# Kernel optimization log

Hardware: AMD Instinct MI355X
Metric: run time of the kernel (lower is better)

The kernel has to match this reference:

```python
import jax, jax.numpy as jnp
import numpy as np

TEMPERATURE = 0.07
EPS = 1e-12  # F.normalize clamp


def _project(x, We, be, W1, b1, W2, b2):
    # encoder Linear then projection head Linear->ReLU->Linear
    h = x @ We + be                      # [B, 512]
    h = jax.nn.relu(h @ W1 + b1)         # [B, 256]
    return h @ W2 + b2                   # [B, 128]


def _ntxent(z1, z2, t):
    B = z1.shape[0]
    z1 = z1 / jnp.maximum(jnp.linalg.norm(z1, axis=1, keepdims=True), EPS)
    z2 = z2 / jnp.maximum(jnp.linalg.norm(z2, axis=1, keepdims=True), EPS)
    reps = jnp.concatenate([z1, z2], axis=0)          # [2B, 128]
    sim = reps @ reps.T                               # [2B, 2B]
    N = 2 * B
    idx = jnp.arange(N)
    # positives: eye rolled by B along columns -> column (i+B) mod N
    pos = sim[idx, (idx + B) % N][:, None]            # [N, 1]
    # negatives: all off-diagonal entries per row, in column order
    cols = jnp.arange(N - 1)[None, :]                 # [1, N-1]
    neg_idx = cols + (cols >= idx[:, None])           # skip the diagonal
    neg = jnp.take_along_axis(sim, neg_idx, axis=1)   # [N, N-1]
    logits = jnp.concatenate([pos, neg], axis=1) / t  # [N, N]
    # cross-entropy with label 0
    return jnp.mean(jax.nn.logsumexp(logits, axis=1) - logits[:, 0])


def setup_inputs() -> dict:
    key = jax.random.key(0)
    ks = jax.random.split(key, 10)
    B, Din, Denc, Dh, Dp = 4096, 1024, 512, 256, 128
    s = lambda fan_in: 1.0 / np.sqrt(fan_in)
    return {
        "x_image": jax.random.normal(ks[0], (B, Din), jnp.float32),
        "x_text": jax.random.normal(ks[1], (B, Din), jnp.float32),
        "We_img": jax.random.normal(ks[2], (Din, Denc), jnp.float32) * s(Din),
        "be_img": jnp.zeros((Denc,), jnp.float32),
        "We_txt": jax.random.normal(ks[3], (Din, Denc), jnp.float32) * s(Din),
        "be_txt": jnp.zeros((Denc,), jnp.float32),
        "Wp1_img": jax.random.normal(ks[4], (Denc, Dh), jnp.float32) * s(Denc),
        "bp1_img": jnp.zeros((Dh,), jnp.float32),
        "Wp2_img": jax.random.normal(ks[5], (Dh, Dp), jnp.float32) * s(Dh),
        "bp2_img": jnp.zeros((Dp,), jnp.float32),
        "Wp1_txt": jax.random.normal(ks[6], (Denc, Dh), jnp.float32) * s(Denc),
        "bp1_txt": jnp.zeros((Dh,), jnp.float32),
        "Wp2_txt": jax.random.normal(ks[7], (Dh, Dp), jnp.float32) * s(Dh),
        "bp2_txt": jnp.zeros((Dp,), jnp.float32),
    }


def reference(x_image, x_text, We_img, be_img, We_txt, be_txt,
              Wp1_img, bp1_img, Wp2_img, bp2_img,
              Wp1_txt, bp1_txt, Wp2_txt, bp2_txt):
    z1 = _project(x_image, We_img, be_img, Wp1_img, bp1_img, Wp2_img, bp2_img)
    z2 = _project(x_text, We_txt, be_txt, Wp1_txt, bp1_txt, Wp2_txt, bp2_txt)
    # single modality pair ('image','text') -> one NT-Xent loss
    return _ntxent(z1, z2, TEMPERATURE)
```

## Files before the change

kernel.cpp:

```cpp
#include <hip/hip_runtime.h>
#include <hip/hip_bf16.h>
#include <math.h>

typedef __bf16 bf16_t;
typedef __bf16 bf8 __attribute__((ext_vector_type(8)));
typedef __bf16 bf4 __attribute__((ext_vector_type(4)));
typedef __bf16 bf16x2 __attribute__((ext_vector_type(2)));
typedef float f32x4 __attribute__((ext_vector_type(4)));

#define AS1 __attribute__((address_space(1)))
#define AS3 __attribute__((address_space(3)))

#define B_ROWS 4096
#define NTOT   8192
#define DIN    1024
#define DENC   512
#define DH     256
#define DP     128
#define NSLICE 16
#define INV_T        14.285714285714286f
#define SCALE_LOG2   20.609929155556620f

__device__ __forceinline__ f32x4 mfma_16x16x32(bf8 a, bf8 b, f32x4 c) {
  return __builtin_amdgcn_mfma_f32_16x16x32_bf16(a, b, c, 0, 0, 0);
}

__global__ __launch_bounds__(256) void prep_kernel(
    const float* __restrict__ x_i, const float* __restrict__ x_t,
    const float* __restrict__ We_i, const float* __restrict__ We_t,
    const float* __restrict__ W1_i, const float* __restrict__ W1_t,
    const float* __restrict__ W2_i, const float* __restrict__ W2_t,
    bf16_t* __restrict__ xb_i, bf16_t* __restrict__ xb_t,
    bf16_t* __restrict__ Wet_i, bf16_t* __restrict__ Wet_t,
    bf16_t* __restrict__ W1t_i, bf16_t* __restrict__ W1t_t,
    bf16_t* __restrict__ W2t_i, bf16_t* __restrict__ W2t_t,
    int* __restrict__ Ctr) {
  const int b = blockIdx.x;
  const int tid = threadIdx.x;
  if (b >= 336) {
    int idx = (b - 336) * 256 + tid;
    const int HALF = (B_ROWS * DIN) / 4;
    const float* s; bf16_t* d; int off;
    if (idx < HALF) { s = x_i; d = xb_i; off = idx; }
    else            { s = x_t; d = xb_t; off = idx - HALF; }
    float4 v = ((const float4*)s)[off];
    bf4 w = { (bf16_t)v.x, (bf16_t)v.y, (bf16_t)v.z, (bf16_t)v.w };
    ((bf4*)d)[off] = w;
    return;
  }
  if (b == 0 && tid < 2) Ctr[tid] = 0;
  const float* src; bf16_t* dst; int K, N, tile;
  if (b < 128)      { src = We_i; dst = Wet_i; K = 1024; N = 512; tile = b; }
  else if (b < 256) { src = We_t; dst = Wet_t; K = 1024; N = 512; tile = b - 128; }
  else if (b < 288) { src = W1_i; dst = W1t_i; K = 512;  N = 256; tile = b - 256; }
  else if (b < 320) { src = W1_t; dst = W1t_t; K = 512;  N = 256; tile = b - 288; }
  else if (b < 328) { src = W2_i; dst = W2t_i; K = 256;  N = 128; tile = b - 320; }
  else              { src = W2_t; dst = W2t_t; K = 256;  N = 128; tile = b - 328; }
  const int tilesN = N >> 6;
  const int k0 = (tile / tilesN) * 64;
  const int n0 = (tile % tilesN) * 64;

  __shared__ float ld[64][65];
  #pragma unroll
  for (int i = 0; i < 4; ++i) {
    int cid = tid + i * 256;
    int r = cid >> 4;
    int c = (cid & 15) * 4;
    float4 v = *(const float4*)(src + (size_t)(k0 + r) * N + n0 + c);
    ld[r][c + 0] = v.x; ld[r][c + 1] = v.y; ld[r][c + 2] = v.z; ld[r][c + 3] = v.w;
  }
  __syncthreads();
  #pragma unroll
  for (int i = 0; i < 2; ++i) {
    int cid = tid + i * 256;
    int rn = cid >> 3;
    int c8 = (cid & 7) * 8;
    bf8 w;
    #pragma unroll
    for (int j = 0; j < 8; ++j) w[j] = (bf16_t)ld[c8 + j][rn];
    *(bf8*)(dst + (size_t)(n0 + rn) * K + k0 + c8) = w;
  }
}

template<int MT, bool RELU>
__global__ __launch_bounds__(256) void gemm_glds(
    const bf16_t* __restrict__ A0, const bf16_t* __restrict__ A1,
    const bf16_t* __restrict__ B0, const bf16_t* __restrict__ B1,
    const float* __restrict__ bias0, const float* __restrict__ bias1,
    bf16_t* __restrict__ out0, bf16_t* __restrict__ out1,
    int N, int K) {
  const bf16_t* A   = blockIdx.z ? A1 : A0;
  const bf16_t* Bt  = blockIdx.z ? B1 : B0;
  const float* bias = blockIdx.z ? bias1 : bias0;
  bf16_t* outp      = blockIdx.z ? out1 : out0;

  const int nb   = blockIdx.x * 64;
  const int mb   = blockIdx.y * MT;
  const int tid  = threadIdx.x;
  const int wave = tid >> 6;
  const int lane = tid & 63;
  const int l15  = lane & 15;
  const int quad = lane >> 4;
  constexpr int CH = MT / 64;

  __shared__ __align__(16) bf16_t As[2][MT * 32];
  __shared__ __align__(16) bf16_t Bs[2][64 * 32];

  f32x4 acc[CH][4];
  #pragma unroll
  for (int i = 0; i < CH; ++i)
    #pragma unroll
    for (int j = 0; j < 4; ++j) acc[i][j] = (f32x4){0.f, 0.f, 0.f, 0.f};

  auto stage = [&](int k0, int pb) {
    #pragma unroll
    for (int i = 0; i < CH; ++i) {
      const int s = tid + i * 256;
      const bf16_t* ga = A + (size_t)(mb + (s >> 2)) * K + k0 + (s & 3) * 8;
      __builtin_amdgcn_global_load_lds(
          (const AS1 void*)ga,
          (AS3 void*)(As[pb] + (size_t)(wave * 64 + i * 256) * 8), 16, 0, 0);
    }
    const bf16_t* gb = Bt + (size_t)(nb + (tid >> 2)) * K + k0 + (tid & 3) * 8;
    __builtin_amdgcn_global_load_lds(
        (const AS1 void*)gb,
        (AS3 void*)(Bs[pb] + (size_t)(wave * 64) * 8), 16, 0, 0);
  };

  stage(0, 0);
  const int T = K >> 5;
  for (int t = 0; t < T; ++t) {
    __syncthreads();
    if (t + 1 < T) stage((t + 1) << 5, (t + 1) & 1);
    const bf16_t* as = As[t & 1];
    const bf16_t* bs = Bs[t & 1];
    bf8 a[CH];
    #pragma unroll
    for (int i = 0; i < CH; ++i)
      a[i] = *(const bf8*)(as + (size_t)(wave * (16 * CH) + i * 16 + l15) * 32 + quad * 8);
    #pragma unroll
    for (int nt = 0; nt < 4; ++nt) {
      bf8 bb = *(const bf8*)(bs + (size_t)(nt * 16 + l15) * 32 + quad * 8);
      #pragma unroll
      for (int i = 0; i < CH; ++i)
        acc[i][nt] = mfma_16x16x32(a[i], bb, acc[i][nt]);
    }
  }

  #pragma unroll
  for (int i = 0; i < CH; ++i) {
    const int orow = mb + wave * (16 * CH) + i * 16 + quad * 4;
    #pragma unroll
    for (int nt = 0; nt < 4; ++nt) {
      const int ocol = nb + nt * 16 + l15;
      const float bval = bias[ocol];
      #pragma unroll
      for (int r = 0; r < 4; ++r) {
        float v = acc[i][nt][r] + bval;
        if (RELU) v = fmaxf(v, 0.f);
        outp[(size_t)(orow + r) * N + ocol] = (bf16_t)v;
      }
    }
  }
}

__global__ __launch_bounds__(256) void head2_norm(
    const bf16_t* __restrict__ A0, const bf16_t* __restrict__ A1,
    const bf16_t* __restrict__ B0, const bf16_t* __restrict__ B1,
    const float* __restrict__ bias0, const float* __restrict__ bias1,
    bf16_t* __restrict__ reps) {
  const bf16_t* A   = blockIdx.z ? A1 : A0;
  const bf16_t* Bt  = blockIdx.z ? B1 : B0;
  const float* bias = blockIdx.z ? bias1 : bias0;

  const int mb   = blockIdx.x * 16;
  const int tid  = threadIdx.x;
  const int wave = tid >> 6;
  const int lane = tid & 63;
  const int l15  = lane & 15;
  const int quad = lane >> 4;
  const int wc0  = wave * 32;

  __shared__ __align__(16) bf16_t Asb[2][16 * 32];
  __shared__ __align__(16) bf16_t Bsb[2][128 * 32];
  __shared__ float ssL[64];

  f32x4 acc[2];
  acc[0] = (f32x4){0.f, 0.f, 0.f, 0.f};
  acc[1] = (f32x4){0.f, 0.f, 0.f, 0.f};

  auto stage = [&](int k0, int pb) {
    if (wave == 0) {
      const int row = lane >> 2, j = lane & 3, cf = j ^ (row & 3);
      const bf16_t* ga = A + (size_t)(mb + row) * DH + k0 + cf * 8;
      __builtin_amdgcn_global_load_lds(
          (const AS1 void*)ga, (AS3 void*)(Asb[pb]), 16, 0, 0);
    }
    #pragma unroll
    for (int i = 0; i < 2; ++i) {
      const int s = wave * 64 + i * 256 + lane;
      const int col = s >> 2, j = s & 3, cf = j ^ (col & 3);
      const bf16_t* gb = Bt + (size_t)col * DH + k0 + cf * 8;
      __builtin_amdgcn_global_load_lds(
          (const AS1 void*)gb,
          (AS3 void*)(Bsb[pb] + (size_t)(wave * 64 + i * 256) * 8), 16, 0, 0);
    }
  };

  stage(0, 0);
  for (int t = 0; t < 8; ++t) {
    __syncthreads();
    if (t < 7) stage((t + 1) << 5, (t + 1) & 1);
    const bf16_t* as = Asb[t & 1];
    const bf16_t* bs = Bsb[t & 1];
    bf8 a = *(const bf8*)(as + (size_t)(l15 * 4 + (quad ^ (l15 & 3))) * 8);
    #pragma unroll
    for (int nt = 0; nt < 2; ++nt) {
      const int col = wc0 + nt * 16 + l15;
      bf8 bb = *(const bf8*)(bs + (size_t)(col * 4 + (quad ^ (col & 3))) * 8);
      acc[nt] = mfma_16x16x32(a, bb, acc[nt]);
    }
  }

  float ssp[4];
  #pragma unroll
  for (int r = 0; r < 4; ++r) {
    #pragma unroll
    for (int nt = 0; nt < 2; ++nt) acc[nt][r] += bias[wc0 + nt * 16 + l15];
    float s = acc[0][r] * acc[0][r] + acc[1][r] * acc[1][r];
    s += __shfl_xor(s, 1); s += __shfl_xor(s, 2);
    s += __shfl_xor(s, 4); s += __shfl_xor(s, 8);
    ssp[r] = s;
  }
  if (l15 == 0) {
    #pragma unroll
    for (int r = 0; r < 4; ++r) ssL[wave * 16 + quad * 4 + r] = ssp[r];
  }
  __syncthreads();
  const size_t gr0 = (size_t)(blockIdx.z ? B_ROWS : 0) + mb + quad * 4;
  #pragma unroll
  for (int r = 0; r < 4; ++r) {
    const int row = quad * 4 + r;
    float tot = ssL[row] + ssL[16 + row] + ssL[32 + row] + ssL[48 + row];
    const float inv = 1.0f / fmaxf(sqrtf(tot), 1e-12f);
    #pragma unroll
    for (int nt = 0; nt < 2; ++nt)
      reps[(gr0 + r) * DP + wc0 + nt * 16 + l15] = (bf16_t)(acc[nt][r] * inv);
  }
}

__global__ __launch_bounds__(256) void sim_rowsum_kernel(
    const bf16_t* __restrict__ reps, float* __restrict__ Spart,
    float* __restrict__ Pos) {
  const int rowbase = blockIdx.y * 128;
  const int slice   = blockIdx.x;
  const int col0    = slice * 512;
  const int tid  = threadIdx.x;
  const int wave = tid >> 6;
  const int lane = tid & 63;
  const int l15  = lane & 15;
  const int quad = lane >> 4;

  __shared__ __align__(16) bf16_t Bs[2][64 * DP];

  const int r0 = rowbase + wave * 32;
  bf8 af0[4], af1[4];
  #pragma unroll
  for (int kt = 0; kt < 4; ++kt) {
    af0[kt] = *(const bf8*)(reps + (size_t)(r0 + l15)      * DP + kt * 32 + quad * 8);
    af1[kt] = *(const bf8*)(reps + (size_t)(r0 + 16 + l15) * DP + kt * 32 + quad * 8);
  }

  float rs0[4] = {0.f, 0.f, 0.f, 0.f};
  float rs1[4] = {0.f, 0.f, 0.f, 0.f};

  auto stage = [&](int t, int pb) {
    const int jt0 = col0 + t * 64;
    #pragma unroll
    for (int r = 0; r < 4; ++r) {
      const int s   = r * 256 + tid;
      const int col = s >> 4;
      const int cf  = (s & 15) ^ (col & 15);
      const bf16_t* g = reps + (size_t)(jt0 + col) * DP + cf * 8;
      __builtin_amdgcn_global_load_lds(
          (const AS1 void*)g,
          (AS3 void*)(Bs[pb] + (size_t)(r * 256 + wave * 64) * 8), 16, 0, 0);
    }
  };

  stage(0, 0);
  for (int t = 0; t < 8; ++t) {
    __syncthreads();
    if (t < 7) stage(t + 1, (t + 1) & 1);
    const bf16_t* buf = Bs[t & 1];
    #pragma unroll
    for (int st = 0; st < 4; ++st) {
      const bf16_t* base = buf + (size_t)(st * 16 + l15) * DP;
      bf8 b0 = *(const bf8*)(base + (((0 * 4 + quad) ^ l15) * 8));
      bf8 b1 = *(const bf8*)(base + (((1 * 4 + quad) ^ l15) * 8));
      bf8 b2 = *(const bf8*)(base + (((2 * 4 + quad) ^ l15) * 8));
      bf8 b3 = *(const bf8*)(base + (((3 * 4 + quad) ^ l15) * 8));
      f32x4 acc0 = (f32x4){0.f, 0.f, 0.f, 0.f};
      f32x4 acc1 = (f32x4){0.f, 0.f, 0.f, 0.f};
      acc0 = mfma_16x16x32(af0[0], b0, acc0); acc1 = mfma_16x16x32(af1[0], b0, acc1);
      acc0 = mfma_16x16x32(af0[1], b1, acc0); acc1 = mfma_16x16x32(af1[1], b1, acc1);
      acc0 = mfma_16x16x32(af0[2], b2, acc0); acc1 = mfma_16x16x32(af1[2], b2, acc1);
      acc0 = mfma_16x16x32(af0[3], b3, acc0); acc1 = mfma_16x16x32(af1[3], b3, acc1);
      #pragma unroll
      for (int r = 0; r < 4; ++r) {
        rs0[r] += __builtin_amdgcn_exp2f(acc0[r] * SCALE_LOG2);
        rs1[r] += __builtin_amdgcn_exp2f(acc1[r] * SCALE_LOG2);
      }
    }
  }

  const bool isDiag = (slice == (rowbase >> 9));
  const bool isPos  = (slice == ((rowbase ^ B_ROWS) >> 9));
  if (isDiag || isPos) {
    #pragma unroll 1
    for (int i = 0; i < 32; ++i) {
      const int row = r0 + i;
      bf16x2 av = *(const bf16x2*)(reps + (size_t)row * DP + lane * 2);
      float a0 = (float)av.x, a1 = (float)av.y;
      float dv;
      if (isDiag) {
        dv = a0 * a0 + a1 * a1;
      } else {
        bf16x2 bv = *(const bf16x2*)(reps + (size_t)(row ^ B_ROWS) * DP + lane * 2);
        dv = a0 * (float)bv.x + a1 * (float)bv.y;
      }
      #pragma unroll
      for (int m = 1; m < 64; m <<= 1) dv += __shfl_xor(dv, m);
      const float e = __builtin_amdgcn_exp2f(dv * SCALE_LOG2);
      const float corr = isDiag ? -e : e;
      const int q = (i & 15) >> 2, r = i & 3;
      if (l15 == 0 && quad == q) {
        if (i < 16) rs0[r] += corr; else rs1[r] += corr;
      }
      if (isPos && lane == 0) Pos[row] = dv;
    }
  }

  const int i0 = r0 + quad * 4;
  #pragma unroll
  for (int r = 0; r < 4; ++r) {
    float v = rs0[r];
    v += __shfl_xor(v, 1); v += __shfl_xor(v, 2);
    v += __shfl_xor(v, 4); v += __shfl_xor(v, 8);
    if (l15 == 0) Spart[(size_t)slice * NTOT + i0 + r] = v;
  }
  #pragma unroll
  for (int r = 0; r < 4; ++r) {
    float v = rs1[r];
    v += __shfl_xor(v, 1); v += __shfl_xor(v, 2);
    v += __shfl_xor(v, 4); v += __shfl_xor(v, 8);
    if (l15 == 0) Spart[(size_t)slice * NTOT + i0 + 16 + r] = v;
  }
}

__global__ __launch_bounds__(256) void rowfinal_kernel(
    const float* __restrict__ Spart, const float* __restrict__ Pos,
    int* __restrict__ cnt, float* __restrict__ Lsum,
    float* __restrict__ out) {
  const int tid = threadIdx.x;
  const int row = blockIdx.x * 256 + tid;
  float s = 0.f;
  #pragma unroll
  for (int k = 0; k < NSLICE; ++k) s += Spart[(size_t)k * NTOT + row];
  float L = logf(s) - Pos[row] * INV_T;
  #pragma unroll
  for (int m = 1; m < 64; m <<= 1) L += __shfl_xor(L, m);
  __shared__ float wpart[4];
  if ((tid & 63) == 0) wpart[tid >> 6] = L;
  __syncthreads();
  if (tid == 0) {
    float bsum = wpart[0] + wpart[1] + wpart[2] + wpart[3];
    atomicAdd(Lsum, bsum);
    __threadfence();
    int old = __hip_atomic_fetch_add(cnt, 1, __ATOMIC_ACQ_REL,
                                     __HIP_MEMORY_SCOPE_AGENT);
    if (old == (int)gridDim.x - 1) {
      float tot = __hip_atomic_load(Lsum, __ATOMIC_RELAXED,
                                    __HIP_MEMORY_SCOPE_AGENT);
      out[0] = tot * (1.0f / NTOT);
    }
  }
}

extern "C" void kernel_launch(void* const* d_in, const int* in_sizes, int n_in,
                              void* d_out, int out_size, void* d_ws, size_t ws_size,
                              hipStream_t stream) {
  const float* x_img  = (const float*)d_in[0];
  const float* x_txt  = (const float*)d_in[1];
  const float* We_img = (const float*)d_in[2];
  const float* be_img = (const float*)d_in[3];
  const float* We_txt = (const float*)d_in[4];
  const float* be_txt = (const float*)d_in[5];
  const float* W1_img = (const float*)d_in[6];
  const float* b1_img = (const float*)d_in[7];
  const float* W2_img = (const float*)d_in[8];
  const float* b2_img = (const float*)d_in[9];
  const float* W1_txt = (const float*)d_in[10];
  const float* b1_txt = (const float*)d_in[11];
  const float* W2_txt = (const float*)d_in[12];
  const float* b2_txt = (const float*)d_in[13];

  char* p = (char*)d_ws;
  bf16_t* xbf_img = (bf16_t*)p; p += (size_t)B_ROWS * DIN * 2;
  bf16_t* xbf_txt = (bf16_t*)p; p += (size_t)B_ROWS * DIN * 2;
  bf16_t* Wet_img = (bf16_t*)p; p += (size_t)DENC * DIN * 2;
  bf16_t* Wet_txt = (bf16_t*)p; p += (size_t)DENC * DIN * 2;
  bf16_t* W1t_img = (bf16_t*)p; p += (size_t)DH * DENC * 2;
  bf16_t* W1t_txt = (bf16_t*)p; p += (size_t)DH * DENC * 2;
  bf16_t* W2t_img = (bf16_t*)p; p += (size_t)DP * DH * 2;
  bf16_t* W2t_txt = (bf16_t*)p; p += (size_t)DP * DH * 2;
  bf16_t* h_img   = (bf16_t*)p; p += (size_t)B_ROWS * DENC * 2;
  bf16_t* h_txt   = (bf16_t*)p; p += (size_t)B_ROWS * DENC * 2;
  bf16_t* g_img   = (bf16_t*)p; p += (size_t)B_ROWS * DH * 2;
  bf16_t* g_txt   = (bf16_t*)p; p += (size_t)B_ROWS * DH * 2;
  bf16_t* reps    = (bf16_t*)p; p += (size_t)NTOT * DP * 2;
  float*  Spart   = (float*) p; p += (size_t)NSLICE * NTOT * 4;
  float*  Pos     = (float*) p; p += (size_t)NTOT * 4;
  int*    Ctr     = (int*)   p; p += 2 * 4;

  prep_kernel<<<336 + 8192, 256, 0, stream>>>(
      x_img, x_txt, We_img, We_txt, W1_img, W1_txt, W2_img, W2_txt,
      xbf_img, xbf_txt, Wet_img, Wet_txt, W1t_img, W1t_txt, W2t_img, W2t_txt,
      Ctr);

  gemm_glds<128, false><<<dim3(DENC / 64, B_ROWS / 128, 2), 256, 0, stream>>>(
      xbf_img, xbf_txt, Wet_img, Wet_txt, be_img, be_txt, h_img, h_txt,
      DENC, DIN);
  gemm_glds<64, true><<<dim3(DH / 64, B_ROWS / 64, 2), 256, 0, stream>>>(
      h_img, h_txt, W1t_img, W1t_txt, b1_img, b1_txt, g_img, g_txt,
      DH, DENC);
  head2_norm<<<dim3(B_ROWS / 16, 1, 2), 256, 0, stream>>>(
      g_img, g_txt, W2t_img, W2t_txt, b2_img, b2_txt, reps);

  sim_rowsum_kernel<<<dim3(NSLICE, NTOT / 128), 256, 0, stream>>>(
      reps, Spart, Pos);
  rowfinal_kernel<<<NTOT / 256, 256, 0, stream>>>(
      Spart, Pos, &Ctr[0], (float*)&Ctr[1], (float*)d_out);
}
```

Before: 187.3 us.

## Enlarge sim tile rows per wave and move diag/pos correction into final kernel

The similarity kernel now gives each wave 64 rows (4 A fragments) instead of 32, so each block covers 256 rows. Every B tile staged in LDS is therefore reused across twice as many MFMAs, and the grid is halved. The diagonal/positive correction and the Pos buffer move out of that kernel: rowfinal now computes them per row with one wave per row. Double buffering is replaced by a single load per step with two barriers, which exposes load latency. The larger A fragment set also raises register pressure.

```diff
diff --git a/kernel.cpp b/kernel.cpp
--- a/kernel.cpp
+++ b/kernel.cpp
@@ -250,9 +250,8 @@
 }
 
 __global__ __launch_bounds__(256) void sim_rowsum_kernel(
-    const bf16_t* __restrict__ reps, float* __restrict__ Spart,
-    float* __restrict__ Pos) {
-  const int rowbase = blockIdx.y * 128;
+    const bf16_t* __restrict__ reps, float* __restrict__ Spart) {
+  const int rowbase = blockIdx.y * 256;
   const int slice   = blockIdx.x;
   const int col0    = slice * 512;
   const int tid  = threadIdx.x;
@@ -263,18 +262,23 @@
 
   __shared__ __align__(16) bf16_t Bs[2][64 * DP];
 
-  const int r0 = rowbase + wave * 32;
-  bf8 af0[4], af1[4];
-  #pragma unroll
-  for (int kt = 0; kt < 4; ++kt) {
-    af0[kt] = *(const bf8*)(reps + (size_t)(r0 + l15)      * DP + kt * 32 + quad * 8);
-    af1[kt] = *(const bf8*)(reps + (size_t)(r0 + 16 + l15) * DP + kt * 32 + quad * 8);
-  }
-
-  float rs0[4] = {0.f, 0.f, 0.f, 0.f};
-  float rs1[4] = {0.f, 0.f, 0.f, 0.f};
-
-  auto stage = [&](int t, int pb) {
+  const int r0 = rowbase + wave * 64;
+  bf8 af[4][4];
+  #pragma unroll
+  for (int c = 0; c < 4; ++c)
+    #pragma unroll
+    for (int kt = 0; kt < 4; ++kt)
+      af[c][kt] = *(const bf8*)(reps + (size_t)(r0 + c * 16 + l15) * DP + kt * 32 + quad * 8);
+
+  float rs[4][4];
+  #pragma unroll
+  for (int c = 0; c < 4; ++c)
+    #pragma unroll
+    for (int r = 0; r < 4; ++r) rs[c][r] = 0.f;
+
+  for (int t = 0; t < 8; ++t) {
+    bf16_t* buf = Bs[t & 1];
+    __syncthreads();
     const int jt0 = col0 + t * 64;
     #pragma unroll
     for (int r = 0; r < 4; ++r) {
@@ -284,15 +288,10 @@
       const bf16_t* g = reps + (size_t)(jt0 + col) * DP + cf * 8;
       __builtin_amdgcn_global_load_lds(
           (const AS1 void*)g,
-          (AS3 void*)(Bs[pb] + (size_t)(r * 256 + wave * 64) * 8), 16, 0, 0);
-    }
-  };
-
-  stage(0, 0);
-  for (int t = 0; t < 8; ++t) {
+          (AS3 void*)(buf + (size_t)(r * 256 + wave * 64) * 8), 16, 0, 0);
+    }
     __syncthreads();
-    if (t < 7) stage(t + 1, (t + 1) & 1);
-    const bf16_t* buf = Bs[t & 1];
+
     #pragma unroll
     for (int st = 0; st < 4; ++st) {
       const bf16_t* base = buf + (size_t)(st * 16 + l15) * DP;
@@ -300,78 +299,60 @@
       bf8 b1 = *(const bf8*)(base + (((1 * 4 + quad) ^ l15) * 8));
       bf8 b2 = *(const bf8*)(base + (((2 * 4 + quad) ^ l15) * 8));
       bf8 b3 = *(const bf8*)(base + (((3 * 4 + quad) ^ l15) * 8));
-      f32x4 acc0 = (f32x4){0.f, 0.f, 0.f, 0.f};
-      f32x4 acc1 = (f32x4){0.f, 0.f, 0.f, 0.f};
-      acc0 = mfma_16x16x32(af0[0], b0, acc0); acc1 = mfma_16x16x32(af1[0], b0, acc1);
-      acc0 = mfma_16x16x32(af0[1], b1, acc0); acc1 = mfma_16x16x32(af1[1], b1, acc1);
-      acc0 = mfma_16x16x32(af0[2], b2, acc0); acc1 = mfma_16x16x32(af1[2], b2, acc1);
-      acc0 = mfma_16x16x32(af0[3], b3, acc0); acc1 = mfma_16x16x32(af1[3], b3, acc1);
       #pragma unroll
-      for (int r = 0; r < 4; ++r) {
-        rs0[r] += __builtin_amdgcn_exp2f(acc0[r] * SCALE_LOG2);
-        rs1[r] += __builtin_amdgcn_exp2f(acc1[r] * SCALE_LOG2);
+      for (int c = 0; c < 4; ++c) {
+        f32x4 acc = (f32x4){0.f, 0.f, 0.f, 0.f};
+        acc = mfma_16x16x32(af[c][0], b0, acc);
+        acc = mfma_16x16x32(af[c][1], b1, acc);
+        acc = mfma_16x16x32(af[c][2], b2, acc);
+        acc = mfma_16x16x32(af[c][3], b3, acc);
+        #pragma unroll
+        for (int r = 0; r < 4; ++r)
+          rs[c][r] += __builtin_amdgcn_exp2f(acc[r] * SCALE_LOG2);
       }
     }
   }
 
-  const bool isDiag = (slice == (rowbase >> 9));
-  const bool isPos  = (slice == ((rowbase ^ B_ROWS) >> 9));
-  if (isDiag || isPos) {
-    #pragma unroll 1
-    for (int i = 0; i < 32; ++i) {
-      const int row = r0 + i;
-      bf16x2 av = *(const bf16x2*)(reps + (size_t)row * DP + lane * 2);
-      float a0 = (float)av.x, a1 = (float)av.y;
-      float dv;
-      if (isDiag) {
-        dv = a0 * a0 + a1 * a1;
-      } else {
-        bf16x2 bv = *(const bf16x2*)(reps + (size_t)(row ^ B_ROWS) * DP + lane * 2);
-        dv = a0 * (float)bv.x + a1 * (float)bv.y;
-      }
-      #pragma unroll
-      for (int m = 1; m < 64; m <<= 1) dv += __shfl_xor(dv, m);
-      const float e = __builtin_amdgcn_exp2f(dv * SCALE_LOG2);
-      const float corr = isDiag ? -e : e;
-      const int q = (i & 15) >> 2, r = i & 3;
-      if (l15 == 0 && quad == q) {
-        if (i < 16) rs0[r] += corr; else rs1[r] += corr;
-      }
-      if (isPos && lane == 0) Pos[row] = dv;
-    }
-  }
-
-  const int i0 = r0 + quad * 4;
-  #pragma unroll
-  for (int r = 0; r < 4; ++r) {
-    float v = rs0[r];
-    v += __shfl_xor(v, 1); v += __shfl_xor(v, 2);
-    v += __shfl_xor(v, 4); v += __shfl_xor(v, 8);
-    if (l15 == 0) Spart[(size_t)slice * NTOT + i0 + r] = v;
-  }
-  #pragma unroll
-  for (int r = 0; r < 4; ++r) {
-    float v = rs1[r];
-    v += __shfl_xor(v, 1); v += __shfl_xor(v, 2);
-    v += __shfl_xor(v, 4); v += __shfl_xor(v, 8);
-    if (l15 == 0) Spart[(size_t)slice * NTOT + i0 + 16 + r] = v;
+  #pragma unroll
+  for (int c = 0; c < 4; ++c) {
+    const int i0 = r0 + c * 16 + quad * 4;
+    #pragma unroll
+    for (int r = 0; r < 4; ++r) {
+      float v = rs[c][r];
+      v += __shfl_xor(v, 1); v += __shfl_xor(v, 2);
+      v += __shfl_xor(v, 4); v += __shfl_xor(v, 8);
+      if (l15 == 0) Spart[(size_t)slice * NTOT + i0 + r] = v;
+    }
   }
 }
 
 __global__ __launch_bounds__(256) void rowfinal_kernel(
-    const float* __restrict__ Spart, const float* __restrict__ Pos,
+    const bf16_t* __restrict__ reps, const float* __restrict__ Spart,
     int* __restrict__ cnt, float* __restrict__ Lsum,
     float* __restrict__ out) {
-  const int tid = threadIdx.x;
-  const int row = blockIdx.x * 256 + tid;
-  float s = 0.f;
-  #pragma unroll
-  for (int k = 0; k < NSLICE; ++k) s += Spart[(size_t)k * NTOT + row];
-  float L = logf(s) - Pos[row] * INV_T;
-  #pragma unroll
-  for (int m = 1; m < 64; m <<= 1) L += __shfl_xor(L, m);
+  const int tid  = threadIdx.x;
+  const int wave = tid >> 6;
+  const int lane = tid & 63;
+  const int row  = blockIdx.x * 4 + wave;
+  bf16x2 a = *(const bf16x2*)(reps + (size_t)row * DP + lane * 2);
+  bf16x2 b = *(const bf16x2*)(reps + (size_t)(row ^ B_ROWS) * DP + lane * 2);
+  float a0 = (float)a.x, a1 = (float)a.y;
+  float b0 = (float)b.x, b1 = (float)b.y;
+  float dii = a0 * a0 + a1 * a1;
+  float pos = a0 * b0 + a1 * b1;
+  float ps  = (lane < NSLICE) ? Spart[(size_t)lane * NTOT + row] : 0.f;
+  #pragma unroll
+  for (int m = 1; m < 64; m <<= 1) {
+    dii += __shfl_xor(dii, m);
+    pos += __shfl_xor(pos, m);
+    ps  += __shfl_xor(ps, m);
+  }
   __shared__ float wpart[4];
-  if ((tid & 63) == 0) wpart[tid >> 6] = L;
+  if (lane == 0) {
+    float Si = ps - __builtin_amdgcn_exp2f(dii * SCALE_LOG2)
+                  + __builtin_amdgcn_exp2f(pos * SCALE_LOG2);
+    wpart[wave] = logf(Si) - pos * INV_T;
+  }
   __syncthreads();
   if (tid == 0) {
     float bsum = wpart[0] + wpart[1] + wpart[2] + wpart[3];
@@ -420,7 +401,6 @@
   bf16_t* g_txt   = (bf16_t*)p; p += (size_t)B_ROWS * DH * 2;
   bf16_t* reps    = (bf16_t*)p; p += (size_t)NTOT * DP * 2;
   float*  Spart   = (float*) p; p += (size_t)NSLICE * NTOT * 4;
-  float*  Pos     = (float*) p; p += (size_t)NTOT * 4;
   int*    Ctr     = (int*)   p; p += 2 * 4;
 
   prep_kernel<<<336 + 8192, 256, 0, stream>>>(
@@ -437,8 +417,7 @@
   head2_norm<<<dim3(B_ROWS / 16, 1, 2), 256, 0, stream>>>(
       g_img, g_txt, W2t_img, W2t_txt, b2_img, b2_txt, reps);
 
-  sim_rowsum_kernel<<<dim3(NSLICE, NTOT / 128), 256, 0, stream>>>(
-      reps, Spart, Pos);
-  rowfinal_kernel<<<NTOT / 256, 256, 0, stream>>>(
-      Spart, Pos, &Ctr[0], (float*)&Ctr[1], (float*)d_out);
-}
+  sim_rowsum_kernel<<<dim3(NSLICE, NTOT / 256), 256, 0, stream>>>(reps, Spart);
+  rowfinal_kernel<<<NTOT / 4, 256, 0, stream>>>(
+      reps, Spart, &Ctr[0], (float*)&Ctr[1], (float*)d_out);
+}
```

Result: slower. 250.8 us (+33.9%).
